# Optimization experiments

Measured on AMD Instinct MI355X. Metric: run time of the kernel, lower is better.

The kernel has to match this reference:

```python
import jax, jax.numpy as jnp
import numpy as np

EPS = 1e-9


def setup_inputs() -> dict:
    key = jax.random.key(0)
    k1, k2, k3, k4 = jax.random.split(key, 4)
    B, D, U = 1024, 512, 512
    x = jax.random.normal(k1, (B, D), dtype=jnp.float32)
    w = jax.random.normal(k2, (D, U), dtype=jnp.float32)
    p = jax.random.normal(k3, (D, U), dtype=jnp.float32)
    b = jax.random.normal(k4, (U,), dtype=jnp.float32)
    return {"x": x, "w": w, "p": p, "b": b}


def reference(x, w, p, b):
    # x: [B, D]; w, p: [D, U]; b: [U]
    xe = x[..., None] + EPS                      # [B, D, 1]
    abs_pow = jnp.abs(xe) ** p                   # [B, D, U]
    is_neg = xe < 0                              # [B, D, 1]
    odd_mask = jnp.mod(p, 2) != 0                # [D, U]
    signed = jnp.where(odd_mask & is_neg, -abs_pow, abs_pow)
    z = jnp.sum(w * signed, axis=1) + b          # [B, U]
    return z  # linear activation
```

## Files before the change

kernel.cpp:

```cpp
#include <hip/hip_runtime.h>
#include <math.h>

#define EPS 1e-9f

constexpr int Bn = 1024, Dn = 512, Un = 512;
constexpr int BM = 64;
constexpr int BU = 64;
constexpr int DK = 16;

typedef float v4f __attribute__((ext_vector_type(4)));

__device__ __forceinline__ int swz(int d) { return ((d >> 2) & 3) << 3; }

template <int SPLITD, bool USE_WS>
__global__ __launch_bounds__(256, 4) void power_layer(
    const float* __restrict__ x, const float* __restrict__ w,
    const float* __restrict__ p, const float* __restrict__ bias,
    float* __restrict__ outp)
{
    constexpr int DPB    = Dn / SPLITD;
    constexpr int NCHUNK = DPB / DK;

    __shared__ float sL[DK][BM];
    __shared__ float sP[DK][BU];
    __shared__ float sW[DK][BU];
    __shared__ float sWX[DK][BU];

    const int tid = threadIdx.x;
    const int tx  = tid & 15;
    const int ty  = tid >> 4;
    const int tx4 = tx * 4;
    const int ty4 = ty * 4;
    const int ub = blockIdx.x * BU;
    const int bb = blockIdx.y * BM;
    const int d0 = blockIdx.z * DPB;

    v4f acc[4] = {};

    for (int ch = 0; ch < NCHUNK; ++ch) {
        const int db = d0 + ch * DK;

        {
            const int r  = tid >> 2;
            const int dq = (tid & 3) << 2;
            const float4 xv = *reinterpret_cast<const float4*>(
                &x[(size_t)(bb + r) * Dn + db + dq]);
            const float* xs = reinterpret_cast<const float*>(&xv);
            #pragma unroll
            for (int j = 0; j < 4; ++j) {
                const float xe = xs[j] + EPS;
                const float La = __builtin_amdgcn_logf(fabsf(xe)) + 64.0f;
                const int dd = dq + j;
                sL[dd][r ^ swz(dd)] = (xe < 0.0f) ? -La : La;
            }
        }
        {
            const int d  = tid >> 4;
            const int uq = (tid & 15) << 2;
            const size_t gi = (size_t)(db + d) * Un + ub + uq;
            const float4 pv = *reinterpret_cast<const float4*>(&p[gi]);
            const float4 wv = *reinterpret_cast<const float4*>(&w[gi]);
            const float* ps  = reinterpret_cast<const float*>(&pv);
            const float* wsv = reinterpret_cast<const float*>(&wv);
            float4 wxv;
            float* wxs = reinterpret_cast<float*>(&wxv);
            #pragma unroll
            for (int j = 0; j < 4; ++j) {
                const bool odd = (fmodf(ps[j], 2.0f) != 0.0f);
                wxs[j] = odd ? -wsv[j] : wsv[j];
            }
            *reinterpret_cast<float4*>(&sP[d][uq])  = pv;
            *reinterpret_cast<float4*>(&sW[d][uq])  = wv;
            *reinterpret_cast<float4*>(&sWX[d][uq]) = wxv;
        }
        __syncthreads();

        #pragma unroll 2
        for (int d = 0; d < DK; ++d) {
            const v4f Lv = *reinterpret_cast<const v4f*>(&sL[d][ty4 ^ swz(d)]);
            const v4f Pv = *reinterpret_cast<const v4f*>(&sP[d][tx4]);
            const v4f Wv = *reinterpret_cast<const v4f*>(&sW[d][tx4]);
            const v4f Xv = *reinterpret_cast<const v4f*>(&sWX[d][tx4]);

            float Ld[4];
            bool  ng[4];
            #pragma unroll
            for (int r = 0; r < 4; ++r) {
                Ld[r] = fabsf(Lv[r]) - 64.0f;
                ng[r] = Lv[r] < 0.0f;
            }

            v4f e[4];
            #pragma unroll
            for (int r = 0; r < 4; ++r) {
                const v4f t = Pv * Ld[r];
                #pragma unroll
                for (int c = 0; c < 4; ++c)
                    e[r][c] = __builtin_amdgcn_exp2f(t[c]);
            }

            #pragma unroll
            for (int r = 0; r < 4; ++r) {
                v4f wsel;
                #pragma unroll
                for (int c = 0; c < 4; ++c)
                    wsel[c] = ng[r] ? Xv[c] : Wv[c];
                acc[r] = __builtin_elementwise_fma(wsel, e[r], acc[r]);
            }
        }
        __syncthreads();
    }

    if (USE_WS) {
        float* dst = outp + ((size_t)blockIdx.z * Bn + bb + ty4) * Un + ub + tx4;
        #pragma unroll
        for (int r = 0; r < 4; ++r)
            *reinterpret_cast<v4f*>(dst + (size_t)r * Un) = acc[r];
    } else {
        if (blockIdx.z == 0) {
            const v4f bv = *reinterpret_cast<const v4f*>(&bias[ub + tx4]);
            #pragma unroll
            for (int r = 0; r < 4; ++r)
                acc[r] += bv;
        }
        #pragma unroll
        for (int r = 0; r < 4; ++r) {
            const int row = bb + ty4 + r;
            #pragma unroll
            for (int c = 0; c < 4; ++c)
                atomicAdd(&outp[(size_t)row * Un + ub + tx4 + c], acc[r][c]);
        }
    }
}

template <int SPLITD>
__global__ __launch_bounds__(256) void reduce_ws(
    const float* __restrict__ ws, const float* __restrict__ bias,
    float* __restrict__ out)
{
    const int nf4 = (Bn * Un) / 4;
    const int i = blockIdx.x * 256 + threadIdx.x;
    if (i >= nf4) return;
    const v4f* w4 = reinterpret_cast<const v4f*>(ws);
    v4f a = w4[i];
    #pragma unroll
    for (int z = 1; z < SPLITD; ++z)
        a += w4[(size_t)z * nf4 + i];
    a += reinterpret_cast<const v4f*>(bias)[i & (Un / 4 - 1)];
    reinterpret_cast<v4f*>(out)[i] = a;
}

extern "C" void kernel_launch(void* const* d_in, const int* in_sizes, int n_in,
                              void* d_out, int out_size, void* d_ws, size_t ws_size,
                              hipStream_t stream) {
    const float* x = (const float*)d_in[0];
    const float* w = (const float*)d_in[1];
    const float* p = (const float*)d_in[2];
    const float* b = (const float*)d_in[3];
    float* out = (float*)d_out;

    const size_t need16 = (size_t)16 * Bn * Un * sizeof(float);
    const size_t need8  = (size_t)8  * Bn * Un * sizeof(float);
    const dim3 blk(256);
    const dim3 rgrid((Bn * Un / 4 + 255) / 256);

    if (ws_size >= need16) {
        float* wsf = (float*)d_ws;
        power_layer<16, true><<<dim3(Un / BU, Bn / BM, 16), blk, 0, stream>>>(x, w, p, b, wsf);
        reduce_ws<16><<<rgrid, blk, 0, stream>>>(wsf, b, out);
    } else if (ws_size >= need8) {
        float* wsf = (float*)d_ws;
        power_layer<8, true><<<dim3(Un / BU, Bn / BM, 8), blk, 0, stream>>>(x, w, p, b, wsf);
        reduce_ws<8><<<rgrid, blk, 0, stream>>>(wsf, b, out);
    } else {
        hipMemsetAsync(out, 0, (size_t)out_size * sizeof(float), stream);
        power_layer<8, false><<<dim3(Un / BU, Bn / BM, 8), blk, 0, stream>>>(x, w, p, b, out);
    }
}
```

Baseline: 106.4 us.

## Fuse split-D reduction into main kernel via last-block counter and prefetch chunks

```diff
diff --git a/kernel.cpp b/kernel.cpp
--- a/kernel.cpp
+++ b/kernel.cpp
@@ -7,16 +7,19 @@
 constexpr int BM = 64;
 constexpr int BU = 64;
 constexpr int DK = 16;
+constexpr int NTILES = (Bn / BM) * (Un / BU);
 
 typedef float v4f __attribute__((ext_vector_type(4)));
 
+__device__ int tile_cnt[NTILES];
+
 __device__ __forceinline__ int swz(int d) { return ((d >> 2) & 3) << 3; }
 
-template <int SPLITD, bool USE_WS>
+template <int SPLITD, int MODE>
 __global__ __launch_bounds__(256, 4) void power_layer(
     const float* __restrict__ x, const float* __restrict__ w,
     const float* __restrict__ p, const float* __restrict__ bias,
-    float* __restrict__ outp)
+    float* __restrict__ outp, float* __restrict__ wsp)
 {
     constexpr int DPB    = Dn / SPLITD;
     constexpr int NCHUNK = DPB / DK;
@@ -35,60 +38,69 @@
     const int bb = blockIdx.y * BM;
     const int d0 = blockIdx.z * DPB;
 
+    const int xr  = tid >> 2;
+    const int xdq = (tid & 3) << 2;
+    const int pd  = tid >> 4;
+    const int puq = (tid & 15) << 2;
+
+    float4 xv, pv, wv;
+
+    auto load_chunk = [&](int ch) {
+        const int db = d0 + ch * DK;
+        xv = *reinterpret_cast<const float4*>(&x[(size_t)(bb + xr) * Dn + db + xdq]);
+        const size_t gi = (size_t)(db + pd) * Un + ub + puq;
+        pv = *reinterpret_cast<const float4*>(&p[gi]);
+        wv = *reinterpret_cast<const float4*>(&w[gi]);
+    };
+
+    auto stage_chunk = [&]() {
+        const float* xs = reinterpret_cast<const float*>(&xv);
+        #pragma unroll
+        for (int j = 0; j < 4; ++j) {
+            const float xe = xs[j] + EPS;
+            const float La = __builtin_amdgcn_logf(fabsf(xe)) + 64.0f;
+            const int dd = xdq + j;
+            sL[dd][xr ^ swz(dd)] = (xe < 0.0f) ? -La : La;
+        }
+        const float* ps  = reinterpret_cast<const float*>(&pv);
+        const float* wsv = reinterpret_cast<const float*>(&wv);
+        float4 wxv;
+        float* wxs = reinterpret_cast<float*>(&wxv);
+        #pragma unroll
+        for (int j = 0; j < 4; ++j) {
+            const bool odd = (fmodf(ps[j], 2.0f) != 0.0f);
+            wxs[j] = odd ? -wsv[j] : wsv[j];
+        }
+        *reinterpret_cast<float4*>(&sP[pd][puq])  = pv;
+        *reinterpret_cast<float4*>(&sW[pd][puq])  = wv;
+        *reinterpret_cast<float4*>(&sWX[pd][puq]) = wxv;
+    };
+
     v4f acc[4] = {};
 
+    load_chunk(0);
+    stage_chunk();
+    __syncthreads();
+
     for (int ch = 0; ch < NCHUNK; ++ch) {
-        const int db = d0 + ch * DK;
-
-        {
-            const int r  = tid >> 2;
-            const int dq = (tid & 3) << 2;
-            const float4 xv = *reinterpret_cast<const float4*>(
-                &x[(size_t)(bb + r) * Dn + db + dq]);
-            const float* xs = reinterpret_cast<const float*>(&xv);
-            #pragma unroll
-            for (int j = 0; j < 4; ++j) {
-                const float xe = xs[j] + EPS;
-                const float La = __builtin_amdgcn_logf(fabsf(xe)) + 64.0f;
-                const int dd = dq + j;
-                sL[dd][r ^ swz(dd)] = (xe < 0.0f) ? -La : La;
-            }
-        }
-        {
-            const int d  = tid >> 4;
-            const int uq = (tid & 15) << 2;
-            const size_t gi = (size_t)(db + d) * Un + ub + uq;
-            const float4 pv = *reinterpret_cast<const float4*>(&p[gi]);
-            const float4 wv = *reinterpret_cast<const float4*>(&w[gi]);
-            const float* ps  = reinterpret_cast<const float*>(&pv);
-            const float* wsv = reinterpret_cast<const float*>(&wv);
-            float4 wxv;
-            float* wxs = reinterpret_cast<float*>(&wxv);
-            #pragma unroll
-            for (int j = 0; j < 4; ++j) {
-                const bool odd = (fmodf(ps[j], 2.0f) != 0.0f);
-                wxs[j] = odd ? -wsv[j] : wsv[j];
-            }
-            *reinterpret_cast<float4*>(&sP[d][uq])  = pv;
-            *reinterpret_cast<float4*>(&sW[d][uq])  = wv;
-            *reinterpret_cast<float4*>(&sWX[d][uq]) = wxv;
-        }
-        __syncthreads();
+        if (ch + 1 < NCHUNK) load_chunk(ch + 1);
 
         #pragma unroll 2
         for (int d = 0; d < DK; ++d) {
             const v4f Lv = *reinterpret_cast<const v4f*>(&sL[d][ty4 ^ swz(d)]);
             const v4f Pv = *reinterpret_cast<const v4f*>(&sP[d][tx4]);
-            const v4f Wv = *reinterpret_cast<const v4f*>(&sW[d][tx4]);
-            const v4f Xv = *reinterpret_cast<const v4f*>(&sWX[d][tx4]);
 
             float Ld[4];
-            bool  ng[4];
+            const float* wp[4];
             #pragma unroll
             for (int r = 0; r < 4; ++r) {
                 Ld[r] = fabsf(Lv[r]) - 64.0f;
-                ng[r] = Lv[r] < 0.0f;
+                wp[r] = (Lv[r] < 0.0f) ? &sWX[d][tx4] : &sW[d][tx4];
             }
+            v4f Wsel[4];
+            #pragma unroll
+            for (int r = 0; r < 4; ++r)
+                Wsel[r] = *reinterpret_cast<const v4f*>(wp[r]);
 
             v4f e[4];
             #pragma unroll
@@ -100,54 +112,70 @@
             }
 
             #pragma unroll
-            for (int r = 0; r < 4; ++r) {
-                v4f wsel;
-                #pragma unroll
-                for (int c = 0; c < 4; ++c)
-                    wsel[c] = ng[r] ? Xv[c] : Wv[c];
-                acc[r] = __builtin_elementwise_fma(wsel, e[r], acc[r]);
-            }
+            for (int r = 0; r < 4; ++r)
+                acc[r] = __builtin_elementwise_fma(Wsel[r], e[r], acc[r]);
         }
         __syncthreads();
-    }
-
-    if (USE_WS) {
-        float* dst = outp + ((size_t)blockIdx.z * Bn + bb + ty4) * Un + ub + tx4;
+        if (ch + 1 < NCHUNK) {
+            stage_chunk();
+            __syncthreads();
+        }
+    }
+
+    if (MODE == 0) {
+        if (blockIdx.z == 0) {
+            const v4f bv = *reinterpret_cast<const v4f*>(&bias[ub + tx4]);
+            #pragma unroll
+            for (int r = 0; r < 4; ++r)
+                acc[r] += bv;
+        }
+        #pragma unroll
+        for (int r = 0; r < 4; ++r) {
+            const int row = bb + ty4 + r;
+            #pragma unroll
+            for (int c = 0; c < 4; ++c)
+                atomicAdd(&outp[(size_t)row * Un + ub + tx4 + c], acc[r][c]);
+        }
+        return;
+    }
+
+    {
+        float* dst = wsp + (((size_t)blockIdx.z * Bn + bb + ty4) * Un + ub + tx4);
         #pragma unroll
         for (int r = 0; r < 4; ++r)
             *reinterpret_cast<v4f*>(dst + (size_t)r * Un) = acc[r];
-    } else {
-        if (blockIdx.z == 0) {
-            const v4f bv = *reinterpret_cast<const v4f*>(&bias[ub + tx4]);
-            #pragma unroll
-            for (int r = 0; r < 4; ++r)
-                acc[r] += bv;
-        }
-        #pragma unroll
-        for (int r = 0; r < 4; ++r) {
-            const int row = bb + ty4 + r;
-            #pragma unroll
-            for (int c = 0; c < 4; ++c)
-                atomicAdd(&outp[(size_t)row * Un + ub + tx4 + c], acc[r][c]);
-        }
-    }
-}
-
-template <int SPLITD>
-__global__ __launch_bounds__(256) void reduce_ws(
-    const float* __restrict__ ws, const float* __restrict__ bias,
-    float* __restrict__ out)
-{
-    const int nf4 = (Bn * Un) / 4;
-    const int i = blockIdx.x * 256 + threadIdx.x;
-    if (i >= nf4) return;
-    const v4f* w4 = reinterpret_cast<const v4f*>(ws);
-    v4f a = w4[i];
+    }
+
+    __threadfence();
+    __syncthreads();
+
+    __shared__ int s_last;
+    if (tid == 0) {
+        const int tile = blockIdx.y * (Un / BU) + blockIdx.x;
+        const int old = __hip_atomic_fetch_add(&tile_cnt[tile], 1,
+                            __ATOMIC_ACQ_REL, __HIP_MEMORY_SCOPE_AGENT);
+        s_last = (old == SPLITD - 1) ? 1 : 0;
+        if (old == SPLITD - 1)
+            __hip_atomic_store(&tile_cnt[tile], 0, __ATOMIC_RELAXED,
+                               __HIP_MEMORY_SCOPE_AGENT);
+    }
+    __syncthreads();
+    if (!s_last) return;
+    __threadfence();
+
+    const v4f bv = *reinterpret_cast<const v4f*>(&bias[ub + tx4]);
+    v4f sum[4] = {bv, bv, bv, bv};
+    const float* srcBase = wsp + ((size_t)(bb + ty4) * Un + ub + tx4);
+    for (int z = 0; z < SPLITD; ++z) {
+        const float* src = srcBase + (size_t)z * Bn * Un;
+        #pragma unroll
+        for (int r = 0; r < 4; ++r)
+            sum[r] += *reinterpret_cast<const v4f*>(src + (size_t)r * Un);
+    }
+    float* dsto = outp + ((size_t)(bb + ty4) * Un + ub + tx4);
     #pragma unroll
-    for (int z = 1; z < SPLITD; ++z)
-        a += w4[(size_t)z * nf4 + i];
-    a += reinterpret_cast<const v4f*>(bias)[i & (Un / 4 - 1)];
-    reinterpret_cast<v4f*>(out)[i] = a;
+    for (int r = 0; r < 4; ++r)
+        *reinterpret_cast<v4f*>(dsto + (size_t)r * Un) = sum[r];
 }
 
 extern "C" void kernel_launch(void* const* d_in, const int* in_sizes, int n_in,
@@ -158,22 +186,18 @@
     const float* p = (const float*)d_in[2];
     const float* b = (const float*)d_in[3];
     float* out = (float*)d_out;
+    float* wsf = (float*)d_ws;
 
     const size_t need16 = (size_t)16 * Bn * Un * sizeof(float);
     const size_t need8  = (size_t)8  * Bn * Un * sizeof(float);
     const dim3 blk(256);
-    const dim3 rgrid((Bn * Un / 4 + 255) / 256);
 
     if (ws_size >= need16) {
-        float* wsf = (float*)d_ws;
-        power_layer<16, true><<<dim3(Un / BU, Bn / BM, 16), blk, 0, stream>>>(x, w, p, b, wsf);
-        reduce_ws<16><<<rgrid, blk, 0, stream>>>(wsf, b, out);
+        power_layer<16, 1><<<dim3(Un / BU, Bn / BM, 16), blk, 0, stream>>>(x, w, p, b, out, wsf);
     } else if (ws_size >= need8) {
-        float* wsf = (float*)d_ws;
-        power_layer<8, true><<<dim3(Un / BU, Bn / BM, 8), blk, 0, stream>>>(x, w, p, b, wsf);
-        reduce_ws<8><<<rgrid, blk, 0, stream>>>(wsf, b, out);
+        power_layer<8, 1><<<dim3(Un / BU, Bn / BM, 8), blk, 0, stream>>>(x, w, p, b, out, wsf);
     } else {
         hipMemsetAsync(out, 0, (size_t)out_size * sizeof(float), stream);
-        power_layer<8, false><<<dim3(Un / BU, Bn / BM, 8), blk, 0, stream>>>(x, w, p, b, out);
+        power_layer<8, 0><<<dim3(Un / BU, Bn / BM, 8), blk, 0, stream>>>(x, w, p, b, out, wsf);
     }
 }
```

Result: slower. 341.5 us (+220.9%).
